# Optimization experiments

Measured on AMD Instinct MI355X. Metric: run time of the kernel, lower is better.

Reference implementation:

```python
import jax, jax.numpy as jnp
import numpy as np

B, C, H, W = 4, 256, 64, 64
CQK = C // 8


def setup_inputs() -> dict:
    key = jax.random.key(0)
    ks = jax.random.split(key, 7)
    s = 1.0 / np.sqrt(C)
    return {
        "x": jax.random.normal(ks[0], (B, C, H, W), dtype=jnp.float32),
        "Wq": jax.random.normal(ks[1], (CQK, C), dtype=jnp.float32) * s,
        "bq": jax.random.normal(ks[2], (CQK,), dtype=jnp.float32) * 0.01,
        "Wk": jax.random.normal(ks[3], (CQK, C), dtype=jnp.float32) * s,
        "bk": jax.random.normal(ks[4], (CQK,), dtype=jnp.float32) * 0.01,
        "Wv": jax.random.normal(ks[5], (C, C), dtype=jnp.float32) * s,
        "bv": jax.random.normal(ks[6], (C,), dtype=jnp.float32) * 0.01,
    }


def reference(x, Wq, bq, Wk, bk, Wv, bv):
    b, c, h, w = x.shape
    n = h * w
    xf = x.reshape(b, c, n)                                   # [B,C,N]
    # 1x1 convs == per-pixel channel projections
    q = jnp.einsum('oc,bcn->bon', Wq, xf) + bq[None, :, None]  # [B,C/8,N]
    k = jnp.einsum('oc,bcn->bon', Wk, xf) + bk[None, :, None]  # [B,C/8,N]
    v = jnp.einsum('oc,bcn->bon', Wv, xf) + bv[None, :, None]  # [B,C,N]
    # energy[b,i,j] = <q[:, i], k[:, j]>  (no scaling, as in the original)
    energy = jnp.einsum('boi,boj->bij', q, k)                  # [B,N,N]
    attn = jax.nn.softmax(energy, axis=-1)                     # [B,N,N]
    # out[b,c,i] = sum_j v[b,c,j] * attn[b,i,j]
    out = jnp.einsum('bcj,bij->bci', v, attn)                  # [B,C,N]
    return out.reshape(b, c, h, w) + x
```

## Files before the change

### kernel.cpp

```cpp
#include <hip/hip_runtime.h>
#include <hip/hip_bf16.h>
#include <math.h>

#define B_DIM 4
#define C_DIM 256
#define CQK_DIM 32
#define N_POS 4096
#define NPART 4

typedef unsigned short u16;
typedef __attribute__((ext_vector_type(8))) short bf16x8;
typedef __attribute__((ext_vector_type(4))) float f32x4;

__device__ __forceinline__ u16 f32_to_bf16_rn(float f) {
    union { float f; unsigned int u; } v; v.f = f;
    unsigned int u = v.u;
    u += 0x7fffu + ((u >> 16) & 1u);
    return (u16)(u >> 16);
}
__device__ __forceinline__ float bf16_to_f32(u16 h) {
    union { unsigned int u; float f; } v; v.u = ((unsigned int)h) << 16;
    return v.f;
}
__device__ __forceinline__ void async_copy16(const u16* g, u16* l) {
    __builtin_amdgcn_global_load_lds(
        (const __attribute__((address_space(1))) void*)g,
        (__attribute__((address_space(3))) void*)l, 16, 0, 0);
}


__global__ __launch_bounds__(256) void proj_kernel(
    const float* __restrict__ x,
    const float* __restrict__ Wq, const float* __restrict__ bq,
    const float* __restrict__ Wk, const float* __restrict__ bk,
    const float* __restrict__ Wv, const float* __restrict__ bv,
    u16* __restrict__ qhi, u16* __restrict__ qlo,
    u16* __restrict__ kth, u16* __restrict__ ktl,
    u16* __restrict__ vtile)
{
    const int t    = threadIdx.x;
    const int blk  = blockIdx.x;
    const int b    = blk >> 6;
    const int jt   = blk & 63;
    const int n0   = jt * 64;
    const int wave = t >> 6;
    const int lane = t & 63;
    const int n16  = lane & 15;
    const int quad = lane >> 4;
    const float* xb = x + (size_t)b * C_DIM * N_POS;

    f32x4 accV[4][4];
    f32x4 accQ[4];
    #pragma unroll
    for (int v = 0; v < 4; ++v)
        #pragma unroll
        for (int nt = 0; nt < 4; ++nt) accV[v][nt] = (f32x4){0.f,0.f,0.f,0.f};
    #pragma unroll
    for (int nt = 0; nt < 4; ++nt) accQ[nt] = (f32x4){0.f,0.f,0.f,0.f};

    const float* Wqk  = (wave < 2) ? Wq : Wk;
    const int    qkrow = (wave & 1) * 16 + n16;

    for (int kk = 0; kk < 8; ++kk) {
        const int k0 = kk * 32 + quad * 8;
        bf16x8 bh[4], bl[4];
        #pragma unroll
        for (int nt = 0; nt < 4; ++nt) {
            const float* xp = xb + (size_t)k0 * N_POS + n0 + nt * 16 + n16;
            float xv[8];
            #pragma unroll
            for (int j = 0; j < 8; ++j) xv[j] = xp[(size_t)j * N_POS];
            #pragma unroll
            for (int j = 0; j < 8; ++j) {
                u16 h = f32_to_bf16_rn(xv[j]);
                bh[nt][j] = (short)h;
                bl[nt][j] = (short)f32_to_bf16_rn(xv[j] - bf16_to_f32(h));
            }
        }
        #pragma unroll
        for (int v = 0; v < 4; ++v) {
            const float* wr = Wv + (size_t)(wave * 64 + v * 16 + n16) * C_DIM + k0;
            float4 a0 = *(const float4*)(wr);
            float4 a1 = *(const float4*)(wr + 4);
            bf16x8 ah;
            ah[0] = (short)f32_to_bf16_rn(a0.x); ah[1] = (short)f32_to_bf16_rn(a0.y);
            ah[2] = (short)f32_to_bf16_rn(a0.z); ah[3] = (short)f32_to_bf16_rn(a0.w);
            ah[4] = (short)f32_to_bf16_rn(a1.x); ah[5] = (short)f32_to_bf16_rn(a1.y);
            ah[6] = (short)f32_to_bf16_rn(a1.z); ah[7] = (short)f32_to_bf16_rn(a1.w);
            #pragma unroll
            for (int nt = 0; nt < 4; ++nt)
                accV[v][nt] = __builtin_amdgcn_mfma_f32_16x16x32_bf16(
                    ah, bh[nt], accV[v][nt], 0, 0, 0);
        }
        {
            const float* wr = Wqk + (size_t)qkrow * C_DIM + k0;
            bf16x8 ah, al;
            #pragma unroll
            for (int j = 0; j < 8; ++j) {
                float w = wr[j];
                u16 h = f32_to_bf16_rn(w);
                ah[j] = (short)h;
                al[j] = (short)f32_to_bf16_rn(w - bf16_to_f32(h));
            }
            #pragma unroll
            for (int nt = 0; nt < 4; ++nt) {
                accQ[nt] = __builtin_amdgcn_mfma_f32_16x16x32_bf16(ah, bh[nt], accQ[nt], 0, 0, 0);
                accQ[nt] = __builtin_amdgcn_mfma_f32_16x16x32_bf16(ah, bl[nt], accQ[nt], 0, 0, 0);
                accQ[nt] = __builtin_amdgcn_mfma_f32_16x16x32_bf16(al, bh[nt], accQ[nt], 0, 0, 0);
            }
        }
    }

    u16* vt = vtile + (size_t)(b * 64 + jt) * (32 * 512);
    #pragma unroll
    for (int v = 0; v < 4; ++v) {
        const int cb = wave * 4 + v;
        #pragma unroll
        for (int r = 0; r < 4; ++r) {
            const int c = cb * 16 + quad * 4 + r;
            const float bias = bv[c];
            #pragma unroll
            for (int nt = 0; nt < 4; ++nt) {
                const int kb = nt >> 1;
                vt[(cb * 2 + kb) * 512
                   + ((n16 >> 2) * 16 + quad * 4 + r) * 8
                   + (nt & 1) * 4 + (n16 & 3)] =
                    f32_to_bf16_rn(accV[v][nt][r] + bias);
            }
        }
    }
    if (wave < 2) {
        #pragma unroll
        for (int r = 0; r < 4; ++r) {
            const int c = (wave & 1) * 16 + quad * 4 + r;
            const float bias = bq[c];
            #pragma unroll
            for (int nt = 0; nt < 4; ++nt) {
                float val = accQ[nt][r] + bias;
                u16 h = f32_to_bf16_rn(val);
                u16 lo = f32_to_bf16_rn(val - bf16_to_f32(h));
                size_t base = ((size_t)b * N_POS + n0 + nt * 16 + n16) * CQK_DIM + c;
                qhi[base] = h; qlo[base] = lo;
            }
        }
    } else {
        u16* kh_t = kth + (size_t)(b * 64 + jt) * (4 * 512);
        u16* kl_t = ktl + (size_t)(b * 64 + jt) * (4 * 512);
        #pragma unroll
        for (int r = 0; r < 4; ++r) {
            const int c = (wave & 1) * 16 + quad * 4 + r;
            const float bias = bk[c];
            #pragma unroll
            for (int nt = 0; nt < 4; ++nt) {
                float val = accQ[nt][r] + bias;
                u16 h = f32_to_bf16_rn(val);
                u16 lo = f32_to_bf16_rn(val - bf16_to_f32(h));
                const int off = nt * 512 + ((c >> 3) * 16 + n16) * 8 + (c & 7);
                kh_t[off] = h; kl_t[off] = lo;
            }
        }
    }
}

__global__ __launch_bounds__(256, 2) void flash_kernel(
    const u16* __restrict__ qhi, const u16* __restrict__ qlo,
    const u16* __restrict__ kth, const u16* __restrict__ ktl,
    const u16* __restrict__ vtile,
    u16* __restrict__ part, float2* __restrict__ ml)
{
    __shared__ u16 Vt[2][32 * 512];

    const int t    = threadIdx.x;
    const int wave = t >> 6;
    const int lane = t & 63;
    const int n16  = lane & 15;
    const int quad = lane >> 4;

    const int idx    = blockIdx.x;
    const int xcd    = idx & 7;
    const int b      = xcd & 3;
    const int z      = idx >> 3;
    const int p      = z & 3;
    const int iouter = z >> 2;
    const int itile  = (iouter << 1) | (xcd >> 2);
    const int i0     = itile * 128 + wave * 32;

    bf16x8 qh[2], ql[2];
    #pragma unroll
    for (int m = 0; m < 2; ++m) {
        qh[m] = *(const bf16x8*)(qhi + ((size_t)b * N_POS + i0 + m * 16 + n16) * CQK_DIM + quad * 8);
        ql[m] = *(const bf16x8*)(qlo + ((size_t)b * N_POS + i0 + m * 16 + n16) * CQK_DIM + quad * 8);
    }

    f32x4 O[2][16];
    #pragma unroll
    for (int m = 0; m < 2; ++m)
        #pragma unroll
        for (int cb = 0; cb < 16; ++cb) O[m][cb] = (f32x4){0.f, 0.f, 0.f, 0.f};
    float lsum[2] = {0.f, 0.f};

    const int jt_beg = p * 16;
    const int jt_end = jt_beg + 16;

    {
        const u16* vsrc = vtile + (size_t)(b * 64 + jt_beg) * (32 * 512);
        for (int ch = wave; ch < 32; ch += 4)
            async_copy16(vsrc + ch * 512 + lane * 8, Vt[0] + ch * 512);
    }

    int buf = 0;
    for (int jt = jt_beg; jt < jt_end; ++jt) {
        const u16* kh_t = kth + (size_t)(b * 64 + jt) * (4 * 512);
        const u16* kl_t = ktl + (size_t)(b * 64 + jt) * (4 * 512);
        bf16x8 kh[4], kl[4];
        #pragma unroll
        for (int jb = 0; jb < 4; ++jb) {
            kh[jb] = *(const bf16x8*)(kh_t + jb * 512 + lane * 8);
            kl[jb] = *(const bf16x8*)(kl_t + jb * 512 + lane * 8);
        }
        __syncthreads();

        if (jt + 1 < jt_end) {
            const u16* vsrc = vtile + (size_t)(b * 64 + jt + 1) * (32 * 512);
            for (int ch = wave; ch < 32; ch += 4)
                async_copy16(vsrc + ch * 512 + lane * 8, Vt[buf ^ 1] + ch * 512);
        }

        f32x4 s[2][4];
        __builtin_amdgcn_s_setprio(1);
        #pragma unroll
        for (int m = 0; m < 2; ++m)
            #pragma unroll
            for (int jb = 0; jb < 4; ++jb) {
                f32x4 acc = (f32x4){0.f, 0.f, 0.f, 0.f};
                acc = __builtin_amdgcn_mfma_f32_16x16x32_bf16(kh[jb], qh[m], acc, 0, 0, 0);
                acc = __builtin_amdgcn_mfma_f32_16x16x32_bf16(kl[jb], qh[m], acc, 0, 0, 0);
                acc = __builtin_amdgcn_mfma_f32_16x16x32_bf16(kh[jb], ql[m], acc, 0, 0, 0);
                s[m][jb] = acc;
            }
        __builtin_amdgcn_s_setprio(0);

        bf16x8 Pf[2][2];
        #pragma unroll
        for (int m = 0; m < 2; ++m)
            #pragma unroll
            for (int jb = 0; jb < 4; ++jb)
                #pragma unroll
                for (int r = 0; r < 4; ++r) {
                    float pv = __expf(s[m][jb][r]);
                    lsum[m] += pv;
                    Pf[m][jb >> 1][(jb & 1) * 4 + r] = (short)f32_to_bf16_rn(pv);
                }

        const u16* vb = Vt[buf];
        __builtin_amdgcn_s_setprio(1);
        #pragma unroll
        for (int kb = 0; kb < 2; ++kb) {
            #pragma unroll
            for (int cb = 0; cb < 16; ++cb) {
                bf16x8 Vf = *(const bf16x8*)(vb + (cb * 2 + kb) * 512 + lane * 8);
                #pragma unroll
                for (int m = 0; m < 2; ++m)
                    O[m][cb] = __builtin_amdgcn_mfma_f32_16x16x32_bf16(
                        Pf[m][kb], Vf, O[m][cb], 0, 0, 0);
            }
        }
        __builtin_amdgcn_s_setprio(0);
        buf ^= 1;
    }

    #pragma unroll
    for (int m = 0; m < 2; ++m) {
        lsum[m] += __shfl_xor(lsum[m], 16, 64);
        lsum[m] += __shfl_xor(lsum[m], 32, 64);
    }
    float inv_l[2][4];
    #pragma unroll
    for (int m = 0; m < 2; ++m)
        #pragma unroll
        for (int r = 0; r < 4; ++r)
            inv_l[m][r] = 1.f / __shfl(lsum[m], quad * 4 + r, 64);

    u16* pbase = part + ((size_t)(p * 4 + b) * N_POS + i0) * C_DIM;
    #pragma unroll
    for (int m = 0; m < 2; ++m)
        #pragma unroll
        for (int cb = 0; cb < 16; ++cb)
            #pragma unroll
            for (int r = 0; r < 4; ++r)
                pbase[(size_t)(m * 16 + quad * 4 + r) * C_DIM + cb * 16 + n16] =
                    f32_to_bf16_rn(O[m][cb][r] * inv_l[m][r]);
    if (quad == 0) {
        #pragma unroll
        for (int m = 0; m < 2; ++m)
            ml[(size_t)(p * 4 + b) * N_POS + i0 + m * 16 + n16] =
                make_float2(0.f, lsum[m]);
    }
}

__global__ __launch_bounds__(256) void reduce_kernel(
    const u16* __restrict__ part, const float2* __restrict__ ml,
    const float* __restrict__ x, float* __restrict__ out)
{
    const int TJ = 32;
    __shared__ float wgt[NPART][TJ];
    __shared__ float trans[C_DIM][TJ + 1];

    const int t   = threadIdx.x;
    const int blk = blockIdx.x;
    const int b   = blk >> 7;
    const int n0  = (blk & 127) * TJ;

    if (t < TJ) {
        int i = n0 + t;
        float s = 0.f, w[NPART];
        #pragma unroll
        for (int p = 0; p < NPART; ++p) {
            float2 a = ml[(size_t)(p * 4 + b) * N_POS + i];
            w[p] = a.y;
            s += w[p];
        }
        float inv = 1.f / s;
        #pragma unroll
        for (int p = 0; p < NPART; ++p) wgt[p][t] = w[p] * inv;
    }
    __syncthreads();

    {
        const int cp = t & 127;
        const int ih = t >> 7;
        for (int ib = 0; ib < TJ; ib += 2) {
            int i = ib + ih;
            float acc0 = 0.f, acc1 = 0.f;
            #pragma unroll
            for (int p = 0; p < NPART; ++p) {
                const u16* row = part + ((size_t)(p * 4 + b) * N_POS + n0 + i) * C_DIM;
                ushort2 pv = ((const ushort2*)row)[cp];
                float wp = wgt[p][i];
                acc0 += wp * bf16_to_f32(pv.x);
                acc1 += wp * bf16_to_f32(pv.y);
            }
            trans[2 * cp][i]     = acc0;
            trans[2 * cp + 1][i] = acc1;
        }
    }
    __syncthreads();

    {
        const int il = t & 31;
        const int cr = t >> 5;
        const float* xb = x + (size_t)b * C_DIM * N_POS;
        float* ob       = out + (size_t)b * C_DIM * N_POS;
        for (int cc = 0; cc < 32; ++cc) {
            int c = cc * 8 + cr;
            size_t g = (size_t)c * N_POS + n0 + il;
            ob[g] = trans[c][il] + xb[g];
        }
    }
}

extern "C" void kernel_launch(void* const* d_in, const int* in_sizes, int n_in,
                              void* d_out, int out_size, void* d_ws, size_t ws_size,
                              hipStream_t stream) {
    const float* x  = (const float*)d_in[0];
    const float* Wq = (const float*)d_in[1];
    const float* bq = (const float*)d_in[2];
    const float* Wk = (const float*)d_in[3];
    const float* bk = (const float*)d_in[4];
    const float* Wv = (const float*)d_in[5];
    const float* bv = (const float*)d_in[6];
    float* out = (float*)d_out;

    char* ws = (char*)d_ws;
    u16*    qhi   = (u16*)(ws);
    u16*    qlo   = (u16*)(ws + (1ull << 20));
    u16*    kth   = (u16*)(ws + (2ull << 20));
    u16*    ktl   = (u16*)(ws + (3ull << 20));
    u16*    vtile = (u16*)(ws + (4ull << 20));
    u16*    part  = (u16*)(ws + (12ull << 20));
    float2* mlp   = (float2*)(ws + (44ull << 20));

    hipLaunchKernelGGL(proj_kernel, dim3(256), dim3(256), 0, stream,
                       x, Wq, bq, Wk, bk, Wv, bv, qhi, qlo, kth, ktl, vtile);
    hipLaunchKernelGGL(flash_kernel, dim3(512), dim3(256), 0, stream,
                       qhi, qlo, kth, ktl, vtile, part, mlp);
    hipLaunchKernelGGL(reduce_kernel, dim3(512), dim3(256), 0, stream,
                       part, mlp, x, out);
}
```

Before: 91.48 us.

## Stream V directly from global into registers and prefetch K in flash loop

```diff
diff --git a/kernel.cpp b/kernel.cpp
--- a/kernel.cpp
+++ b/kernel.cpp
@@ -22,10 +22,10 @@
     union { unsigned int u; float f; } v; v.u = ((unsigned int)h) << 16;
     return v.f;
 }
-__device__ __forceinline__ void async_copy16(const u16* g, u16* l) {
-    __builtin_amdgcn_global_load_lds(
-        (const __attribute__((address_space(1))) void*)g,
-        (__attribute__((address_space(3))) void*)l, 16, 0, 0);
+__device__ __forceinline__ unsigned pk_bf16(float a, float b) {
+    unsigned r;
+    asm("v_cvt_pk_bf16_f32 %0, %1, %2" : "=v"(r) : "v"(a), "v"(b));
+    return r;
 }
 
 
@@ -168,8 +168,6 @@
     const u16* __restrict__ vtile,
     u16* __restrict__ part, float2* __restrict__ ml)
 {
-    __shared__ u16 Vt[2][32 * 512];
-
     const int t    = threadIdx.x;
     const int wave = t >> 6;
     const int lane = t & 63;
@@ -202,29 +200,30 @@
     const int jt_beg = p * 16;
     const int jt_end = jt_beg + 16;
 
+    const u16* vb_base = vtile + (size_t)b * 64 * (32 * 512);
+    const u16* kh_base = kth   + (size_t)b * 64 * (4 * 512);
+    const u16* kl_base = ktl   + (size_t)b * 64 * (4 * 512);
+
+    bf16x8 kh[4], kl[4];
     {
-        const u16* vsrc = vtile + (size_t)(b * 64 + jt_beg) * (32 * 512);
-        for (int ch = wave; ch < 32; ch += 4)
-            async_copy16(vsrc + ch * 512 + lane * 8, Vt[0] + ch * 512);
-    }
-
-    int buf = 0;
-    for (int jt = jt_beg; jt < jt_end; ++jt) {
-        const u16* kh_t = kth + (size_t)(b * 64 + jt) * (4 * 512);
-        const u16* kl_t = ktl + (size_t)(b * 64 + jt) * (4 * 512);
-        bf16x8 kh[4], kl[4];
+        const u16* kh_t = kh_base + (size_t)jt_beg * (4 * 512);
+        const u16* kl_t = kl_base + (size_t)jt_beg * (4 * 512);
         #pragma unroll
         for (int jb = 0; jb < 4; ++jb) {
             kh[jb] = *(const bf16x8*)(kh_t + jb * 512 + lane * 8);
             kl[jb] = *(const bf16x8*)(kl_t + jb * 512 + lane * 8);
         }
-        __syncthreads();
-
-        if (jt + 1 < jt_end) {
-            const u16* vsrc = vtile + (size_t)(b * 64 + jt + 1) * (32 * 512);
-            for (int ch = wave; ch < 32; ch += 4)
-                async_copy16(vsrc + ch * 512 + lane * 8, Vt[buf ^ 1] + ch * 512);
-        }
+    }
+    bf16x8 Vbuf[4];
+    {
+        const u16* vt0 = vb_base + (size_t)jt_beg * (32 * 512);
+        #pragma unroll
+        for (int f = 0; f < 4; ++f)
+            Vbuf[f] = *(const bf16x8*)(vt0 + f * 512 + lane * 8);
+    }
+
+    for (int jt = jt_beg; jt < jt_end; ++jt) {
+        __builtin_amdgcn_s_barrier();
 
         f32x4 s[2][4];
         __builtin_amdgcn_s_setprio(1);
@@ -240,33 +239,55 @@
             }
         __builtin_amdgcn_s_setprio(0);
 
+        {
+            const int jn = (jt + 1 < jt_end) ? jt + 1 : jt_beg;
+            const u16* kh_t = kh_base + (size_t)jn * (4 * 512);
+            const u16* kl_t = kl_base + (size_t)jn * (4 * 512);
+            #pragma unroll
+            for (int jb = 0; jb < 4; ++jb) {
+                kh[jb] = *(const bf16x8*)(kh_t + jb * 512 + lane * 8);
+                kl[jb] = *(const bf16x8*)(kl_t + jb * 512 + lane * 8);
+            }
+        }
+
         bf16x8 Pf[2][2];
         #pragma unroll
         for (int m = 0; m < 2; ++m)
             #pragma unroll
-            for (int jb = 0; jb < 4; ++jb)
+            for (int kb = 0; kb < 2; ++kb) {
+                union { bf16x8 v; unsigned u[4]; } tmp;
                 #pragma unroll
-                for (int r = 0; r < 4; ++r) {
-                    float pv = __expf(s[m][jb][r]);
-                    lsum[m] += pv;
-                    Pf[m][jb >> 1][(jb & 1) * 4 + r] = (short)f32_to_bf16_rn(pv);
+                for (int j2 = 0; j2 < 2; ++j2) {
+                    const int jb = kb * 2 + j2;
+                    float p0 = __expf(s[m][jb][0]);
+                    float p1 = __expf(s[m][jb][1]);
+                    float p2 = __expf(s[m][jb][2]);
+                    float p3 = __expf(s[m][jb][3]);
+                    lsum[m] += (p0 + p1) + (p2 + p3);
+                    tmp.u[j2 * 2 + 0] = pk_bf16(p0, p1);
+                    tmp.u[j2 * 2 + 1] = pk_bf16(p2, p3);
                 }
-
-        const u16* vb = Vt[buf];
+                Pf[m][kb] = tmp.v;
+            }
+
+        const u16* vcur = vb_base + (size_t)jt * (32 * 512);
+        const u16* vnxt = vb_base + (size_t)((jt + 1 < jt_end) ? jt + 1 : jt_beg) * (32 * 512);
         __builtin_amdgcn_s_setprio(1);
         #pragma unroll
-        for (int kb = 0; kb < 2; ++kb) {
-            #pragma unroll
-            for (int cb = 0; cb < 16; ++cb) {
-                bf16x8 Vf = *(const bf16x8*)(vb + (cb * 2 + kb) * 512 + lane * 8);
-                #pragma unroll
-                for (int m = 0; m < 2; ++m)
-                    O[m][cb] = __builtin_amdgcn_mfma_f32_16x16x32_bf16(
-                        Pf[m][kb], Vf, O[m][cb], 0, 0, 0);
-            }
+        for (int f = 0; f < 32; ++f) {
+            const int cb = f >> 1;
+            const int kb = f & 1;
+            bf16x8 Vf = Vbuf[f & 3];
+            const int fn = f + 4;
+            const u16* src = (fn < 32) ? (vcur + fn * 512 + lane * 8)
+                                       : (vnxt + (fn - 32) * 512 + lane * 8);
+            Vbuf[f & 3] = *(const bf16x8*)src;
+            #pragma unroll
+            for (int m = 0; m < 2; ++m)
+                O[m][cb] = __builtin_amdgcn_mfma_f32_16x16x32_bf16(
+                    Pf[m][kb], Vf, O[m][cb], 0, 0, 0);
         }
         __builtin_amdgcn_s_setprio(0);
-        buf ^= 1;
     }
 
     #pragma unroll
```

After: 135.3 us. 47.9% more time.

## Stage K tiles through LDS with async copies and pack bf16 conversions

Applied to the files above, without the earlier changes.

```diff
diff --git a/kernel.cpp b/kernel.cpp
--- a/kernel.cpp
+++ b/kernel.cpp
@@ -21,6 +21,11 @@
 __device__ __forceinline__ float bf16_to_f32(u16 h) {
     union { unsigned int u; float f; } v; v.u = ((unsigned int)h) << 16;
     return v.f;
+}
+__device__ __forceinline__ unsigned pk_bf16(float a, float b) {
+    unsigned r;
+    asm("v_cvt_pk_bf16_f32 %0, %1, %2" : "=v"(r) : "v"(a), "v"(b));
+    return r;
 }
 __device__ __forceinline__ void async_copy16(const u16* g, u16* l) {
     __builtin_amdgcn_global_load_lds(
@@ -168,7 +173,7 @@
     const u16* __restrict__ vtile,
     u16* __restrict__ part, float2* __restrict__ ml)
 {
-    __shared__ u16 Vt[2][32 * 512];
+    __shared__ u16 Vt[2][40 * 512];
 
     const int t    = threadIdx.x;
     const int wave = t >> 6;
@@ -202,28 +207,37 @@
     const int jt_beg = p * 16;
     const int jt_end = jt_beg + 16;
 
-    {
-        const u16* vsrc = vtile + (size_t)(b * 64 + jt_beg) * (32 * 512);
-        for (int ch = wave; ch < 32; ch += 4)
-            async_copy16(vsrc + ch * 512 + lane * 8, Vt[0] + ch * 512);
-    }
+    const u16* vb_base = vtile + (size_t)b * 64 * (32 * 512);
+    const u16* kh_base = kth   + (size_t)b * 64 * (4 * 512);
+    const u16* kl_base = ktl   + (size_t)b * 64 * (4 * 512);
+
+#define STAGE(JT, BUF)                                                          \
+    {                                                                           \
+        const u16* vsrc  = vb_base + (size_t)(JT) * (32 * 512);                 \
+        const u16* khsrc = kh_base + (size_t)(JT) * (4 * 512);                  \
+        const u16* klsrc = kl_base + (size_t)(JT) * (4 * 512);                  \
+        for (int ch = wave; ch < 32; ch += 4)                                   \
+            async_copy16(vsrc + ch * 512 + lane * 8, Vt[BUF] + ch * 512);       \
+        for (int ch = wave; ch < 8; ch += 4)                                    \
+            async_copy16((ch < 4 ? khsrc + ch * 512 : klsrc + (ch - 4) * 512)   \
+                             + lane * 8,                                        \
+                         Vt[BUF] + (32 + ch) * 512);                            \
+    }
+
+    STAGE(jt_beg, 0);
 
     int buf = 0;
     for (int jt = jt_beg; jt < jt_end; ++jt) {
-        const u16* kh_t = kth + (size_t)(b * 64 + jt) * (4 * 512);
-        const u16* kl_t = ktl + (size_t)(b * 64 + jt) * (4 * 512);
+        __syncthreads();
+
+        if (jt + 1 < jt_end) STAGE(jt + 1, buf ^ 1);
+
+        const u16* kbuf = Vt[buf];
         bf16x8 kh[4], kl[4];
         #pragma unroll
         for (int jb = 0; jb < 4; ++jb) {
-            kh[jb] = *(const bf16x8*)(kh_t + jb * 512 + lane * 8);
-            kl[jb] = *(const bf16x8*)(kl_t + jb * 512 + lane * 8);
-        }
-        __syncthreads();
-
-        if (jt + 1 < jt_end) {
-            const u16* vsrc = vtile + (size_t)(b * 64 + jt + 1) * (32 * 512);
-            for (int ch = wave; ch < 32; ch += 4)
-                async_copy16(vsrc + ch * 512 + lane * 8, Vt[buf ^ 1] + ch * 512);
+            kh[jb] = *(const bf16x8*)(kbuf + (32 + jb) * 512 + lane * 8);
+            kl[jb] = *(const bf16x8*)(kbuf + (36 + jb) * 512 + lane * 8);
         }
 
         f32x4 s[2][4];
@@ -244,13 +258,21 @@
         #pragma unroll
         for (int m = 0; m < 2; ++m)
             #pragma unroll
-            for (int jb = 0; jb < 4; ++jb)
+            for (int kb = 0; kb < 2; ++kb) {
+                union { bf16x8 v; unsigned u[4]; } tmp;
                 #pragma unroll
-                for (int r = 0; r < 4; ++r) {
-                    float pv = __expf(s[m][jb][r]);
-                    lsum[m] += pv;
-                    Pf[m][jb >> 1][(jb & 1) * 4 + r] = (short)f32_to_bf16_rn(pv);
+                for (int j2 = 0; j2 < 2; ++j2) {
+                    const int jb = kb * 2 + j2;
+                    float p0 = __expf(s[m][jb][0]);
+                    float p1 = __expf(s[m][jb][1]);
+                    float p2 = __expf(s[m][jb][2]);
+                    float p3 = __expf(s[m][jb][3]);
+                    lsum[m] += (p0 + p1) + (p2 + p3);
+                    tmp.u[j2 * 2 + 0] = pk_bf16(p0, p1);
+                    tmp.u[j2 * 2 + 1] = pk_bf16(p2, p3);
                 }
+                Pf[m][kb] = tmp.v;
+            }
 
         const u16* vb = Vt[buf];
         __builtin_amdgcn_s_setprio(1);
@@ -268,6 +290,7 @@
         __builtin_amdgcn_s_setprio(0);
         buf ^= 1;
     }
+#undef STAGE
 
     #pragma unroll
     for (int m = 0; m < 2; ++m) {
```

Measured after the change: 88.51 us. 3.2% less time.
